# Kernel tuning notes

Hardware: AMD Instinct MI355X
Metric: run time of the kernel (lower is better)

Reference implementation:

```python
import jax, jax.numpy as jnp
import numpy as np

N_USER, N_ITEM, N_ENT = 60000, 30000, 15000
E_UI, E_IE = 1_000_000, 300_000
DIM, FACTOR_K, DIM_K, ITERS = 50, 2, 25, 4
INDEX = [(0, 1), (1, 0)] + [(1, j) for j in range(2, 8)]
I_LIST = [[0], [1, 2, 3, 4, 5, 6, 7]]


def _l2n(x):
    # F.normalize(p=2, dim=2), eps=1e-12
    return x / jnp.clip(jnp.linalg.norm(x, axis=2, keepdims=True), 1e-12)


def _forward(edges, embs_in, Wtk, at, W, q_rela):
    n_types = len(embs_in)
    # fac(): project each node type into factor_k subspaces [k, n, dim_k]
    embs = [_l2n(jax.nn.leaky_relu(jnp.einsum('nd,kde->kne', embs_in[i], Wtk[i]), 0.2))
            for i in range(n_types)]
    rows = [embs[a].shape[1] for (a, b) in INDEX]
    # r_rela init: uniform over factors, never fed back (as in the source)
    r_node = [jnp.full((FACTOR_K, rows[e]), 1.0 / FACTOR_K, dtype=embs[0].dtype)
              for e in range(len(INDEX))]

    def rela_update(edge, new_emb, old_emb, a, r_n, n_rows, q_r):
        u, col = edge[0], edge[1]
        # edge gather + attention score per factor: [k, E]
        ui = jnp.concatenate([new_emb[:, u], old_emb[:, col]], axis=2)  # [k,E,2*dk]
        e_ts_k = jax.nn.relu(jnp.einsum('ked,kd->ke', ui, a))
        vals = jnp.sum(e_ts_k * r_n[:, u], axis=0)  # [E]
        # sparse row-wise softmax (torch.sparse.softmax dim=1)
        m = jax.ops.segment_max(vals, u, num_segments=n_rows)
        ex = jnp.exp(vals - m[u])
        attn = ex / jax.ops.segment_sum(ex, u, num_segments=n_rows)[u]
        # sparse mm per factor: scatter attn-weighted neighbor features
        msg = attn[None, :, None] * old_emb[:, col]  # [k,E,dk]
        z = jax.vmap(lambda mk: jax.ops.segment_sum(mk, u, num_segments=n_rows))(msg)
        z = jnp.einsum('kne,ef->knf', jax.nn.leaky_relu(z, 0.2), W)
        r = jax.nn.softmax(jnp.einsum('kne,e->kn', jnp.tanh(z), q_r), axis=0)
        return r, z

    # note: in the source all_new_emb aliases all_ego_emb (same list), so updates persist
    for _ in range(ITERS):
        rl, el = [], []
        for e in range(len(INDEX)):
            a_i, b_i = INDEX[e]
            r, z = rela_update(edges[e], embs[a_i], embs[b_i], at[e], r_node[e], rows[e], q_rela[e])
            rl.append(r)
            el.append(z)
        for i in range(2):
            ego = embs[i]
            for j in I_LIST[i]:
                ego = ego + el[j] * rl[j][:, :, None]
            embs[i] = _l2n(ego)

    def flat(e):  # torch.cat(list(e), dim=1): [k,n,d] -> [n, k*d]
        k, n, d = e.shape
        return jnp.transpose(e, (1, 0, 2)).reshape(n, k * d)

    return jnp.concatenate([flat(embs[0]), flat(embs[1])], axis=0)


def setup_inputs() -> dict:
    key = jax.random.key(0)
    ks = jax.random.split(key, 40)
    inp = {}

    def edges(k1, k2, E, nr, nc):
        r = jax.random.randint(k1, (E,), 0, nr)
        c = jax.random.randint(k2, (E,), 0, nc)
        return jnp.stack([r, c]).astype(jnp.int32)

    inp['edge0'] = edges(ks[0], ks[1], E_UI, N_USER, N_ITEM)
    inp['edge1'] = edges(ks[2], ks[3], E_UI, N_ITEM, N_USER)
    for e in range(2, 8):
        inp[f'edge{e}'] = edges(ks[2 * e], ks[2 * e + 1], E_IE, N_ITEM, N_ENT)
    sizes = [N_USER, N_ITEM] + [N_ENT] * 6
    for i, n in enumerate(sizes):
        inp[f'emb{i}'] = jax.random.normal(ks[16 + i], (n, DIM), jnp.float32) * 0.1
    inp['Wtk'] = jax.random.normal(ks[30], (8, FACTOR_K, DIM, DIM_K), jnp.float32) * (2.0 / (DIM + DIM_K)) ** 0.5
    inp['at'] = jax.random.normal(ks[31], (8, FACTOR_K, 2 * DIM_K), jnp.float32) * 0.1
    inp['W'] = jax.random.normal(ks[32], (DIM_K, DIM_K), jnp.float32) * 0.2
    inp['q_rela'] = jax.random.normal(ks[33], (8, DIM_K), jnp.float32) * 0.2
    return inp


def reference(edge0, edge1, edge2, edge3, edge4, edge5, edge6, edge7,
              emb0, emb1, emb2, emb3, emb4, emb5, emb6, emb7,
              Wtk, at, W, q_rela):
    edges = [edge0, edge1, edge2, edge3, edge4, edge5, edge6, edge7]
    embs_in = [emb0, emb1, emb2, emb3, emb4, emb5, emb6, emb7]
    return _forward(edges, embs_in, Wtk, at, W, q_rela)
```

## Files before the change

kernel.cpp:

```cpp
#include <hip/hip_runtime.h>
#include <math.h>


#define KF 2
#define DK 25
#define DD 50
#define PS 52
#define ITERS 4
#define WPB 4

static __device__ __forceinline__ float leakyf(float x) { return x > 0.f ? x : 0.2f * x; }

static __device__ __forceinline__ float2 score_row50(const float* p, const float* a) {
    float s0 = 0.f, s1 = 0.f;
    #pragma unroll
    for (int f = 0; f < DK; ++f) {
        s0 = fmaf(p[f],      a[f],      s0);
        s1 = fmaf(p[DK + f], a[50 + f], s1);
    }
    return make_float2(s0, s1);
}
static __device__ __forceinline__ float2 score_col50(const float* p, const float* a) {
    float s0 = 0.f, s1 = 0.f;
    #pragma unroll
    for (int f = 0; f < DK; ++f) {
        s0 = fmaf(p[f],      a[25 + f], s0);
        s1 = fmaf(p[DK + f], a[75 + f], s1);
    }
    return make_float2(s0, s1);
}

struct FacArgs { const float* emb[8]; float* P[8]; const float* Wtk; int base[9]; };

__global__ void fac_kernel(FacArgs A) {
    int g = blockIdx.x * blockDim.x + threadIdx.x;
    if (g >= A.base[8]) return;
    int ty = 0;
    while (g >= A.base[ty + 1]) ++ty;
    int node = g - A.base[ty];
    const float* er = A.emb[ty] + (size_t)node * DD;
    const float* Wt = A.Wtk + (size_t)ty * KF * DD * DK;
    float x[DD];
    #pragma unroll
    for (int d = 0; d < DD; ++d) x[d] = er[d];
    float out[DD];
    #pragma unroll
    for (int k = 0; k < KF; ++k) {
        const float* Wk = Wt + k * DD * DK;
        float nrm = 0.f;
        for (int f = 0; f < DK; ++f) {
            float acc = 0.f;
            for (int d = 0; d < DD; ++d) acc = fmaf(x[d], Wk[d * DK + f], acc);
            acc = leakyf(acc);
            out[k * DK + f] = acc;
            nrm = fmaf(acc, acc, nrm);
        }
        float inv = 1.f / fmaxf(sqrtf(nrm), 1e-12f);
        for (int f = 0; f < DK; ++f) out[k * DK + f] *= inv;
    }
    float* Pr = A.P[ty] + (size_t)node * PS;
    #pragma unroll
    for (int j = 0; j < DD; ++j) Pr[j] = out[j];
    Pr[50] = 0.f; Pr[51] = 0.f;
}

struct EdgeArgs {
    const int* rows[8]; const int* cols[8];
    int* cnt;
    unsigned short* colind;
    int ebase[9];
    int rowbase[8];
};

__global__ void hist_kernel(EdgeArgs A) {
    int g = blockIdx.x * blockDim.x + threadIdx.x;
    if (g >= A.ebase[8]) return;
    int rel = 0;
    while (g >= A.ebase[rel + 1]) ++rel;
    int e = g - A.ebase[rel];
    atomicAdd(&A.cnt[A.rowbase[rel] + A.rows[rel][e]], 1);
}

__global__ __launch_bounds__(1024) void scan_part_kernel(int* a, int n, int* bsum) {
    __shared__ int lds[1024];
    int tid = threadIdx.x;
    int i = blockIdx.x * 1024 + tid;
    int v = (i < n) ? a[i] : 0;
    lds[tid] = v;
    __syncthreads();
    int x = v;
    for (int off = 1; off < 1024; off <<= 1) {
        int y = (tid >= off) ? lds[tid - off] : 0;
        __syncthreads();
        x += y;
        lds[tid] = x;
        __syncthreads();
    }
    if (i < n) a[i] = x - v;
    if (tid == 1023) bsum[blockIdx.x] = x;
}

__global__ __launch_bounds__(1024) void scan_bsum_kernel(int* bsum, int nb) {
    __shared__ int lds[1024];
    int tid = threadIdx.x;
    int v = (tid < nb) ? bsum[tid] : 0;
    lds[tid] = v;
    __syncthreads();
    int x = v;
    for (int off = 1; off < 1024; off <<= 1) {
        int y = (tid >= off) ? lds[tid - off] : 0;
        __syncthreads();
        x += y;
        lds[tid] = x;
        __syncthreads();
    }
    if (tid < nb) bsum[tid] = x - v;
}

__global__ __launch_bounds__(1024) void add_off_kernel(int* a, int n, const int* bsum) {
    int i = blockIdx.x * 1024 + threadIdx.x;
    if (i < n) a[i] += bsum[blockIdx.x];
}

__global__ void scatter_kernel(EdgeArgs A) {
    int g = blockIdx.x * blockDim.x + threadIdx.x;
    if (g >= A.ebase[8]) return;
    int rel = 0;
    while (g >= A.ebase[rel + 1]) ++rel;
    int e = g - A.ebase[rel];
    int p = atomicAdd(&A.cnt[A.rowbase[rel] + A.rows[rel][e]], 1);
    A.colind[p] = (unsigned short)A.cols[rel][e];
}

struct SbArgs { const float* Pb[6]; const float* at[6]; float2* sb[6]; int base[7]; };

__global__ void sb_kernel(SbArgs A) {
    int g = blockIdx.x * blockDim.x + threadIdx.x;
    if (g >= A.base[6]) return;
    int rel = 0;
    while (g >= A.base[rel + 1]) ++rel;
    int c = g - A.base[rel];
    const float* p = A.Pb[rel] + (size_t)c * PS;
    A.sb[rel][c] = score_col50(p, A.at[rel]);
}

struct ScoreArgs {
    const float* P0; const float* P1;
    const float* at;
    float2* sa[8]; float2* sb0; float2* sb1;
    int n0, n1;
};

__global__ void score01_kernel(ScoreArgs A) {
    int g = blockIdx.x * blockDim.x + threadIdx.x;
    if (g >= A.n0 + A.n1) return;
    if (g < A.n0) {
        const float* p = A.P0 + (size_t)g * PS;
        float pr[DD];
        #pragma unroll
        for (int j = 0; j < DD; ++j) pr[j] = p[j];
        A.sa[0][g] = score_row50(pr, A.at + 0);
        A.sb1[g]   = score_col50(pr, A.at + 100);
    } else {
        int node = g - A.n0;
        const float* p = A.P1 + (size_t)node * PS;
        float pr[DD];
        #pragma unroll
        for (int j = 0; j < DD; ++j) pr[j] = p[j];
        #pragma unroll
        for (int e = 1; e < 8; ++e) A.sa[e][node] = score_row50(pr, A.at + e * 100);
        A.sb0[node] = score_col50(pr, A.at + 0);
    }
}

struct PhaseArgs {
    const int* rowptr;
    const unsigned short* colind;
    const float* Pb[8];
    const float* q[8];
    const float2* sa[8]; const float2* sb[8];
    float* z[8]; float* r[8];
    const float* W;
    int rowbase[9];
};

__global__ __launch_bounds__(WPB * 64) void phase_kernel(PhaseArgs A, int totalRows) {
    int wave = blockIdx.x * WPB + (threadIdx.x >> 6);
    int lane = threadIdx.x & 63;
    if (wave >= totalRows) return;
    int rel = 0;
    while (wave >= A.rowbase[rel + 1]) ++rel;
    int u = wave - A.rowbase[rel];

    const unsigned short* colind = A.colind;
    const float* Pb = A.Pb[rel];
    const float* qv = A.q[rel];
    const float2* sb = A.sb[rel];
    float2 h = A.sa[rel][u];
    int beg = wave ? A.rowptr[wave - 1] : 0;
    int end = A.rowptr[wave];

    bool act = lane < DD;
    int grp4 = lane >> 4, sub4 = lane & 15;
    float ssum = 0.f;
    float4 a4 = make_float4(0.f, 0.f, 0.f, 0.f);

    for (int base = beg; base < end; base += 64) {
        int idx = base + lane;
        bool vld = idx < end;
        int cb = vld ? (int)colind[idx] : 0;
        float evl = 0.f;
        if (vld) {
            float2 sc = sb[cb];
            evl = __expf(0.5f * (fmaxf(h.x + sc.x, 0.f) + fmaxf(h.y + sc.y, 0.f)));
        }
        ssum += evl;
        int nb = min(64, end - base);
        #pragma unroll 2
        for (int t = 0; t < nb; t += 4) {
            int srcl = t + grp4;
            int c = __shfl(cb, srcl);
            float ev = __shfl(evl, srcl);
            const float4* pc = (const float4*)(Pb + (size_t)c * PS);
            float4 v = pc[sub4];
            a4.x = fmaf(ev, v.x, a4.x);
            a4.y = fmaf(ev, v.y, a4.y);
            a4.z = fmaf(ev, v.z, a4.z);
            a4.w = fmaf(ev, v.w, a4.w);
        }
    }
    #pragma unroll
    for (int off = 32; off >= 16; off >>= 1) {
        a4.x += __shfl_xor(a4.x, off);
        a4.y += __shfl_xor(a4.y, off);
        a4.z += __shfl_xor(a4.z, off);
        a4.w += __shfl_xor(a4.w, off);
    }
    #pragma unroll
    for (int off = 32; off; off >>= 1) ssum += __shfl_xor(ssum, off);

    int src = lane >> 2;
    float fx = __shfl(a4.x, src), fy = __shfl(a4.y, src);
    float fz = __shfl(a4.z, src), fw = __shfl(a4.w, src);
    float za = (lane & 1) ? ((lane & 2) ? fw : fy) : ((lane & 2) ? fz : fx);

    float inv = (ssum > 0.f) ? (1.f / ssum) : 0.f;
    float zl = act ? leakyf(za * inv) : 0.f;

    int fcol = act ? ((lane < DK) ? lane : (lane - DK)) : 0;
    int kbase = (act && lane >= DK) ? DK : 0;
    float o = 0.f;
    const float* W = A.W;
    #pragma unroll
    for (int d = 0; d < DK; ++d) {
        float zd = __shfl(zl, kbase + d);
        o = fmaf(zd, W[d * DK + fcol], o);
    }
    float th = act ? tanhf(o) * qv[fcol] : 0.f;
    float t0 = (lane < DK) ? th : 0.f;
    float t1 = th - t0;
    #pragma unroll
    for (int off = 32; off; off >>= 1) { t0 += __shfl_xor(t0, off); t1 += __shfl_xor(t1, off); }
    float m = fmaxf(t0, t1);
    float e0 = __expf(t0 - m), e1 = __expf(t1 - m);
    float rinv = 1.f / (e0 + e1);

    if (act) A.z[rel][(size_t)u * DD + lane] = o;
    if (lane == 0) {
        A.r[rel][(size_t)u * 2 + 0] = e0 * rinv;
        A.r[rel][(size_t)u * 2 + 1] = e1 * rinv;
    }
}

static __device__ __forceinline__ void l2norm_store(float* dst, const float* acc) {
    #pragma unroll
    for (int k = 0; k < KF; ++k) {
        float nrm = 0.f;
        for (int f = 0; f < DK; ++f) nrm = fmaf(acc[k * DK + f], acc[k * DK + f], nrm);
        float inv = 1.f / fmaxf(sqrtf(nrm), 1e-12f);
        for (int f = 0; f < DK; ++f) dst[k * DK + f] = acc[k * DK + f] * inv;
    }
}

struct EgoArgs { float* P0; float* P1; const float* zz[8]; const float* rr[8]; int n0, n1; };

__global__ void ego_kernel(EgoArgs A) {
    int g = blockIdx.x * blockDim.x + threadIdx.x;
    if (g >= A.n0 + A.n1) return;
    float acc[DD];
    if (g < A.n0) {
        float* Pr = A.P0 + (size_t)g * PS;
        const float* zr = A.zz[0] + (size_t)g * DD;
        float r0 = A.rr[0][(size_t)g * 2], r1 = A.rr[0][(size_t)g * 2 + 1];
        #pragma unroll
        for (int j = 0; j < DD; ++j) acc[j] = fmaf(zr[j], (j < DK ? r0 : r1), Pr[j]);
        l2norm_store(Pr, acc);
    } else {
        int node = g - A.n0;
        float* Pr = A.P1 + (size_t)node * PS;
        #pragma unroll
        for (int j = 0; j < DD; ++j) acc[j] = Pr[j];
        for (int e = 1; e < 8; ++e) {
            const float* zr = A.zz[e] + (size_t)node * DD;
            float r0 = A.rr[e][(size_t)node * 2], r1 = A.rr[e][(size_t)node * 2 + 1];
            #pragma unroll
            for (int j = 0; j < DD; ++j) acc[j] = fmaf(zr[j], (j < DK ? r0 : r1), acc[j]);
        }
        l2norm_store(Pr, acc);
    }
}

__global__ void out_kernel(const float* __restrict__ P0, const float* __restrict__ P1,
                           int n0, int n1, float* __restrict__ out) {
    int g = blockIdx.x * blockDim.x + threadIdx.x;
    if (g >= n0 + n1) return;
    const float* src = (g < n0) ? (P0 + (size_t)g * PS) : (P1 + (size_t)(g - n0) * PS);
    float* dst = out + (size_t)g * DD;
    #pragma unroll
    for (int j = 0; j < DD; ++j) dst[j] = src[j];
}

static inline int cdiv(int a, int b) { return (a + b - 1) / b; }

extern "C" void kernel_launch(void* const* d_in, const int* in_sizes, int n_in,
                              void* d_out, int out_size, void* d_ws, size_t ws_size,
                              hipStream_t stream) {
    const int* edge[8];
    int E[8];
    for (int e = 0; e < 8; ++e) { edge[e] = (const int*)d_in[e]; E[e] = in_sizes[e] / 2; }
    const float* emb[8];
    int nn[8];
    for (int i = 0; i < 8; ++i) { emb[i] = (const float*)d_in[8 + i]; nn[i] = in_sizes[8 + i] / DD; }
    const float* Wtk = (const float*)d_in[16];
    const float* at  = (const float*)d_in[17];
    const float* W   = (const float*)d_in[18];
    const float* q   = (const float*)d_in[19];
    float* out = (float*)d_out;

    static const int aIdx[8] = {0, 1, 1, 1, 1, 1, 1, 1};
    static const int bIdx[8] = {1, 0, 2, 3, 4, 5, 6, 7};
    int rows[8], ncol[8];
    for (int e = 0; e < 8; ++e) { rows[e] = nn[aIdx[e]]; ncol[e] = nn[bIdx[e]]; }
    int rowbase[9];
    rowbase[0] = 0;
    for (int e = 0; e < 8; ++e) rowbase[e + 1] = rowbase[e] + rows[e];
    int totalRows = rowbase[8];
    int ebase[9];
    ebase[0] = 0;
    for (int e = 0; e < 8; ++e) ebase[e + 1] = ebase[e] + E[e];
    int totE = ebase[8];

    char* w = (char*)d_ws;
    size_t off = 0;
    auto alloc_f  = [&](size_t n) { float*  p = (float*)(w + off);  off += n * 4; return p; };
    auto alloc_f2 = [&](size_t n) { float2* p = (float2*)(w + off); off += n * 8; return p; };
    auto alloc_i  = [&](size_t n) { int*    p = (int*)(w + off);    off += n * 4; return p; };
    float* P[8]; for (int i = 0; i < 8; ++i) P[i] = alloc_f((size_t)nn[i] * PS);
    float* z[8]; for (int e = 0; e < 8; ++e) z[e] = alloc_f((size_t)rows[e] * DD);
    float* r[8]; for (int e = 0; e < 8; ++e) r[e] = alloc_f((size_t)rows[e] * 2);
    float2* sb[8]; for (int e = 0; e < 8; ++e) sb[e] = alloc_f2((size_t)ncol[e]);
    float2* sa[8]; for (int e = 0; e < 8; ++e) sa[e] = alloc_f2((size_t)rows[e]);
    int* cnt = alloc_i((size_t)totalRows);
    int nchunks = cdiv(totalRows, 1024);
    int* bsum = alloc_i((size_t)nchunks);
    unsigned short* colind = (unsigned short*)(w + off);
    off += (size_t)totE * 2;
    (void)ws_size;

    const int B = 256;

    hipMemsetAsync(cnt, 0, (size_t)totalRows * 4, stream);
    EdgeArgs EA;
    for (int e = 0; e < 8; ++e) {
        EA.rows[e] = edge[e]; EA.cols[e] = edge[e] + E[e];
        EA.rowbase[e] = rowbase[e];
        EA.ebase[e] = ebase[e];
    }
    EA.ebase[8] = ebase[8];
    EA.cnt = cnt; EA.colind = colind;
    hist_kernel<<<cdiv(totE, B), B, 0, stream>>>(EA);
    scan_part_kernel<<<nchunks, 1024, 0, stream>>>(cnt, totalRows, bsum);
    scan_bsum_kernel<<<1, 1024, 0, stream>>>(bsum, nchunks);
    add_off_kernel<<<nchunks, 1024, 0, stream>>>(cnt, totalRows, bsum);
    scatter_kernel<<<cdiv(totE, B), B, 0, stream>>>(EA);

    FacArgs FA;
    FA.base[0] = 0;
    for (int i = 0; i < 8; ++i) { FA.emb[i] = emb[i]; FA.P[i] = P[i]; FA.base[i + 1] = FA.base[i] + nn[i]; }
    FA.Wtk = Wtk;
    fac_kernel<<<cdiv(FA.base[8], B), B, 0, stream>>>(FA);

    SbArgs SBs;
    SBs.base[0] = 0;
    for (int e = 2; e < 8; ++e) {
        SBs.Pb[e - 2] = P[bIdx[e]];
        SBs.at[e - 2] = at + (size_t)e * KF * DD;
        SBs.sb[e - 2] = sb[e];
        SBs.base[e - 1] = SBs.base[e - 2] + ncol[e];
    }
    sb_kernel<<<cdiv(SBs.base[6], B), B, 0, stream>>>(SBs);

    ScoreArgs SC;
    SC.P0 = P[0]; SC.P1 = P[1]; SC.at = at;
    for (int e = 0; e < 8; ++e) SC.sa[e] = sa[e];
    SC.sb0 = sb[0]; SC.sb1 = sb[1];
    SC.n0 = nn[0]; SC.n1 = nn[1];
    score01_kernel<<<cdiv(nn[0] + nn[1], B), B, 0, stream>>>(SC);

    PhaseArgs PA;
    PA.rowptr = cnt; PA.colind = colind;
    for (int e = 0; e < 8; ++e) {
        PA.Pb[e] = P[bIdx[e]];
        PA.q[e]  = q + (size_t)e * DK;
        PA.sa[e] = sa[e]; PA.sb[e] = sb[e];
        PA.z[e] = z[e]; PA.r[e] = r[e];
        PA.rowbase[e] = rowbase[e];
    }
    PA.rowbase[8] = rowbase[8];
    PA.W = W;
    EgoArgs GA;
    GA.P0 = P[0]; GA.P1 = P[1]; GA.n0 = nn[0]; GA.n1 = nn[1];
    for (int e = 0; e < 8; ++e) { GA.zz[e] = z[e]; GA.rr[e] = r[e]; }

    for (int it = 0; it < ITERS; ++it) {
        phase_kernel<<<cdiv(totalRows, WPB), WPB * 64, 0, stream>>>(PA, totalRows);
        ego_kernel<<<cdiv(nn[0] + nn[1], B), B, 0, stream>>>(GA);
        score01_kernel<<<cdiv(nn[0] + nn[1], B), B, 0, stream>>>(SC);
    }

    out_kernel<<<cdiv(nn[0] + nn[1], B), B, 0, stream>>>(P[0], P[1], nn[0], nn[1], out);
}
```

Measured before the change: 1.747 ms.

## Move W projection and factor softmax epilogue from phase kernel into ego kernel

The per-row epilogue (leaky_relu, 25x25 W projection, tanh·q reduction, two-way softmax) moves out of the wave-per-row phase kernel, which now stores only the normalized aggregate. The ego kernel recomputes that epilogue per node in a single thread before accumulating, which removes the r buffer writes and reads along with the shuffle-heavy reductions in the phase kernel. In exchange the ego kernel does serial per-thread matmuls (up to 7 relations per item node) with large register arrays, risking spills and low occupancy. The inner gather loop unroll also rises from 2 to 4.

Result: slower. 3.734 ms (+113.7%).

```diff
diff --git a/kernel.cpp b/kernel.cpp
--- a/kernel.cpp
+++ b/kernel.cpp
@@ -177,10 +177,8 @@
     const int* rowptr;
     const unsigned short* colind;
     const float* Pb[8];
-    const float* q[8];
     const float2* sa[8]; const float2* sb[8];
-    float* z[8]; float* r[8];
-    const float* W;
+    float* z[8];
     int rowbase[9];
 };
 
@@ -194,7 +192,6 @@
 
     const unsigned short* colind = A.colind;
     const float* Pb = A.Pb[rel];
-    const float* qv = A.q[rel];
     const float2* sb = A.sb[rel];
     float2 h = A.sa[rel][u];
     int beg = wave ? A.rowptr[wave - 1] : 0;
@@ -216,7 +213,7 @@
         }
         ssum += evl;
         int nb = min(64, end - base);
-        #pragma unroll 2
+        #pragma unroll 4
         for (int t = 0; t < nb; t += 4) {
             int srcl = t + grp4;
             int c = __shfl(cb, srcl);
@@ -245,31 +242,30 @@
     float za = (lane & 1) ? ((lane & 2) ? fw : fy) : ((lane & 2) ? fz : fx);
 
     float inv = (ssum > 0.f) ? (1.f / ssum) : 0.f;
-    float zl = act ? leakyf(za * inv) : 0.f;
-
-    int fcol = act ? ((lane < DK) ? lane : (lane - DK)) : 0;
-    int kbase = (act && lane >= DK) ? DK : 0;
-    float o = 0.f;
-    const float* W = A.W;
-    #pragma unroll
-    for (int d = 0; d < DK; ++d) {
-        float zd = __shfl(zl, kbase + d);
-        o = fmaf(zd, W[d * DK + fcol], o);
-    }
-    float th = act ? tanhf(o) * qv[fcol] : 0.f;
-    float t0 = (lane < DK) ? th : 0.f;
-    float t1 = th - t0;
-    #pragma unroll
-    for (int off = 32; off; off >>= 1) { t0 += __shfl_xor(t0, off); t1 += __shfl_xor(t1, off); }
+    if (act) A.z[rel][(size_t)u * DD + lane] = za * inv;
+}
+
+static __device__ __forceinline__ void epi_rel(const float* zraw, const float* W,
+                                               const float* qv, float* o, float2* rr) {
+    float zi[DD];
+    #pragma unroll
+    for (int j = 0; j < DD; ++j) zi[j] = leakyf(zraw[j]);
+    float t0 = 0.f, t1 = 0.f;
+    #pragma unroll
+    for (int k = 0; k < KF; ++k) {
+        float tk = 0.f;
+        for (int f = 0; f < DK; ++f) {
+            float acc = 0.f;
+            for (int d = 0; d < DK; ++d) acc = fmaf(zi[k * DK + d], W[d * DK + f], acc);
+            o[k * DK + f] = acc;
+            tk = fmaf(tanhf(acc), qv[f], tk);
+        }
+        if (k == 0) t0 = tk; else t1 = tk;
+    }
     float m = fmaxf(t0, t1);
     float e0 = __expf(t0 - m), e1 = __expf(t1 - m);
     float rinv = 1.f / (e0 + e1);
-
-    if (act) A.z[rel][(size_t)u * DD + lane] = o;
-    if (lane == 0) {
-        A.r[rel][(size_t)u * 2 + 0] = e0 * rinv;
-        A.r[rel][(size_t)u * 2 + 1] = e1 * rinv;
-    }
+    *rr = make_float2(e0 * rinv, e1 * rinv);
 }
 
 static __device__ __forceinline__ void l2norm_store(float* dst, const float* acc) {
@@ -282,18 +278,26 @@
     }
 }
 
-struct EgoArgs { float* P0; float* P1; const float* zz[8]; const float* rr[8]; int n0, n1; };
+struct EgoArgs {
+    float* P0; float* P1;
+    const float* zz[8];
+    const float* W; const float* q;
+    int n0, n1;
+};
 
 __global__ void ego_kernel(EgoArgs A) {
     int g = blockIdx.x * blockDim.x + threadIdx.x;
     if (g >= A.n0 + A.n1) return;
-    float acc[DD];
+    float acc[DD], o[DD], zraw[DD];
+    float2 rr;
     if (g < A.n0) {
         float* Pr = A.P0 + (size_t)g * PS;
         const float* zr = A.zz[0] + (size_t)g * DD;
-        float r0 = A.rr[0][(size_t)g * 2], r1 = A.rr[0][(size_t)g * 2 + 1];
-        #pragma unroll
-        for (int j = 0; j < DD; ++j) acc[j] = fmaf(zr[j], (j < DK ? r0 : r1), Pr[j]);
+        #pragma unroll
+        for (int j = 0; j < DD; ++j) zraw[j] = zr[j];
+        epi_rel(zraw, A.W, A.q + 0, o, &rr);
+        #pragma unroll
+        for (int j = 0; j < DD; ++j) acc[j] = fmaf(o[j], (j < DK ? rr.x : rr.y), Pr[j]);
         l2norm_store(Pr, acc);
     } else {
         int node = g - A.n0;
@@ -302,9 +306,11 @@
         for (int j = 0; j < DD; ++j) acc[j] = Pr[j];
         for (int e = 1; e < 8; ++e) {
             const float* zr = A.zz[e] + (size_t)node * DD;
-            float r0 = A.rr[e][(size_t)node * 2], r1 = A.rr[e][(size_t)node * 2 + 1];
             #pragma unroll
-            for (int j = 0; j < DD; ++j) acc[j] = fmaf(zr[j], (j < DK ? r0 : r1), acc[j]);
+            for (int j = 0; j < DD; ++j) zraw[j] = zr[j];
+            epi_rel(zraw, A.W, A.q + e * DK, o, &rr);
+            #pragma unroll
+            for (int j = 0; j < DD; ++j) acc[j] = fmaf(o[j], (j < DK ? rr.x : rr.y), acc[j]);
         }
         l2norm_store(Pr, acc);
     }
@@ -357,7 +363,6 @@
     auto alloc_i  = [&](size_t n) { int*    p = (int*)(w + off);    off += n * 4; return p; };
     float* P[8]; for (int i = 0; i < 8; ++i) P[i] = alloc_f((size_t)nn[i] * PS);
     float* z[8]; for (int e = 0; e < 8; ++e) z[e] = alloc_f((size_t)rows[e] * DD);
-    float* r[8]; for (int e = 0; e < 8; ++e) r[e] = alloc_f((size_t)rows[e] * 2);
     float2* sb[8]; for (int e = 0; e < 8; ++e) sb[e] = alloc_f2((size_t)ncol[e]);
     float2* sa[8]; for (int e = 0; e < 8; ++e) sa[e] = alloc_f2((size_t)rows[e]);
     int* cnt = alloc_i((size_t)totalRows);
@@ -411,16 +416,15 @@
     PA.rowptr = cnt; PA.colind = colind;
     for (int e = 0; e < 8; ++e) {
         PA.Pb[e] = P[bIdx[e]];
-        PA.q[e]  = q + (size_t)e * DK;
         PA.sa[e] = sa[e]; PA.sb[e] = sb[e];
-        PA.z[e] = z[e]; PA.r[e] = r[e];
+        PA.z[e] = z[e];
         PA.rowbase[e] = rowbase[e];
     }
     PA.rowbase[8] = rowbase[8];
-    PA.W = W;
     EgoArgs GA;
     GA.P0 = P[0]; GA.P1 = P[1]; GA.n0 = nn[0]; GA.n1 = nn[1];
-    for (int e = 0; e < 8; ++e) { GA.zz[e] = z[e]; GA.rr[e] = r[e]; }
+    for (int e = 0; e < 8; ++e) GA.zz[e] = z[e];
+    GA.W = W; GA.q = q;
 
     for (int it = 0; it < ITERS; ++it) {
         phase_kernel<<<cdiv(totalRows, WPB), WPB * 64, 0, stream>>>(PA, totalRows);
```
